# Kernel optimization log

Hardware: AMD Instinct MI355X
Metric: run time of the kernel (lower is better)

The kernel has to match this reference:

```python
import jax, jax.numpy as jnp
import numpy as np
from jax import lax

PI = jnp.pi
KX = jnp.array([[-1, 0, 1], [-2, 0, 2], [-1, 0, 1]], jnp.float32)
KY = jnp.array([[-1, -2, -1], [0, 0, 0], [1, 2, 1]], jnp.float32)
K45 = jnp.array([[-2, -1, 0], [-1, 0, 1], [0, 1, 2]], jnp.float32)
K135 = jnp.array([[0, 1, 2], [-1, 0, 1], [-2, -1, 0]], jnp.float32)


def _shift(x, dx, dy):
    # result[i, j] = x[clip(i - dx), clip(j - dy)]  (replicate boundary),
    # exactly matching the torch slice + replicate-pad neighbor construction.
    H, W = x.shape[2], x.shape[3]
    ri = jnp.clip(jnp.arange(H) - dx, 0, H - 1)
    ci = jnp.clip(jnp.arange(W) - dy, 0, W - 1)
    return x[:, :, ri[:, None], ci[None, :]]


def _adaptive_smoothing(f, k=10.0, iter_num=3):
    neighbors = [(-1, -1), (-1, 0), (-1, 1), (0, -1), (0, 0), (0, 1), (1, -1), (1, 0), (1, 1)]
    for _ in range(iter_num):
        Gx = (_shift(f, -1, 0) - _shift(f, 1, 0)) * 0.5   # gradient along H
        Gy = (_shift(f, 0, -1) - _shift(f, 0, 1)) * 0.5   # gradient along W
        w = jnp.exp(-(Gx * Gx + Gy * Gy) / (2.0 * k * k))
        f_new = jnp.zeros_like(f)
        w_sum = jnp.zeros_like(f)
        for dx, dy in neighbors:
            f_new = f_new + _shift(f, dx, dy) * _shift(w, dx, dy)
            w_sum = w_sum + _shift(w, dx, dy)
        f = f_new / jnp.maximum(w_sum, 1e-8)
    return f


def _dwconv(x, k2d):
    # depthwise 3x3 cross-correlation, zero padding (torch Conv2d semantics)
    C = x.shape[1]
    kern = jnp.broadcast_to(k2d[None, None], (C, 1, 3, 3)).astype(x.dtype)
    return lax.conv_general_dilated(x, kern, (1, 1), ((1, 1), (1, 1)),
                                    dimension_numbers=('NCHW', 'OIHW', 'NCHW'),
                                    feature_group_count=C)


def _sobel(x):
    return 0.5 * jnp.abs(_dwconv(x, KX)) + 0.5 * jnp.abs(_dwconv(x, KY))


def _hardswish(x):
    return x * jnp.clip(x + 3.0, 0.0, 6.0) / 6.0


def _canny(data, sigma, weight):
    blurred = _adaptive_smoothing(data, k=10.0, iter_num=3)
    sob = _sobel(blurred)
    B, C, H, W = sob.shape
    # torch.median: lower median = sorted[(n-1)//2]; .item() detaches it
    flat = jnp.sort(sob.reshape(B, C, H * W), axis=-1)
    med = lax.stop_gradient(jnp.mean(flat[:, :, (H * W - 1) // 2]))
    low = jnp.clip((1.0 - sigma) * med, 0.001, 1.0)
    high = jnp.clip((1.0 + sigma) * med, 0.001, 1.0)

    ex = _dwconv(blurred, KX)
    ey = _dwconv(blurred, KY)
    e45 = _dwconv(blurred, K45)
    e135 = _dwconv(blurred, K135)
    mag = jnp.sqrt(ex * ex + ey * ey + e45 * e45 + e135 * e135)
    ang = jnp.mod(jnp.arctan2(ey, ex), PI)

    dirs = jnp.array([0.0, PI / 4, PI / 2, 3 * PI / 4], jnp.float32)
    d = jnp.abs(ang[..., None] - dirs)
    dir_w = jax.nn.softmax(-jnp.minimum(d, PI - d) / 0.01, axis=-1)  # (B,C,H,W,4)

    pm = jnp.pad(mag, ((0, 0), (0, 0), (1, 1), (1, 1)), mode='edge')
    neigh = [(pm[:, :, 1:-1, :-2], pm[:, :, 1:-1, 2:]),
             (pm[:, :, :-2, :-2], pm[:, :, 2:, 2:]),
             (pm[:, :, :-2, 1:-1], pm[:, :, 2:, 1:-1]),
             (pm[:, :, :-2, 2:], pm[:, :, 2:, :-2])]
    sup = jnp.zeros_like(mag)
    for i, (n1, n2) in enumerate(neigh):  # fixed 4-direction loop
        sw = jax.nn.softmax(jnp.stack([mag, n1, n2], axis=-1) / 0.1, axis=-1)[..., 0]
        sup = sup + mag * sw * dir_w[..., i]

    mx = jnp.max(sup)
    sup = sup / jnp.where(mx > 0, mx, 1.0)

    Sh = _hardswish(sup - high)
    Sl = _hardswish(sup - low)
    ecanny = sup * (Sh + Sl)
    dilated = _dwconv(Sh, jnp.ones((3, 3), jnp.float32))
    result = ecanny + dilated * Sl * (1.0 - Sh)

    # enhance_edges with the ORIGINAL input
    result = (1.0 - weight) * result + weight * _sobel(data)
    rmin = jnp.min(result)
    rmax = jnp.max(result)
    return (result - rmin) / (rmax - rmin)


def setup_inputs() -> dict:
    key = jax.random.key(0)
    k1, k2 = jax.random.split(key)
    B, C, H, W = 8, 1, 512, 512
    return {
        'img1': jax.random.uniform(k1, (B, C, H, W), dtype=jnp.float32),
        'img2': jax.random.uniform(k2, (B, C, H, W), dtype=jnp.float32),
        'sigma1': jnp.float32(2.2),
        'enhance_weight1': jnp.float32(0.0),
        'sigma2': jnp.float32(2.2),
        'enhance_weight2': jnp.float32(0.0),
    }


def reference(img1, img2, sigma1, enhance_weight1, sigma2, enhance_weight2):
    s1 = 1.0 - jax.nn.sigmoid(sigma1)
    w1 = jax.nn.sigmoid(enhance_weight1)
    s2 = 1.0 - jax.nn.sigmoid(sigma2)
    w2 = jax.nn.sigmoid(enhance_weight2)
    m1 = _canny(img1, s1, w1)
    m2 = _canny(img2, s2, w2)
    f = (1.0 - m1) * (1.0 - m2) + m1 * m2
    return (1.0 - f, m1, m2)
```

## Files before the change

kernel.cpp:

```cpp
#include <hip/hip_runtime.h>

namespace {

constexpr int H = 512;
constexpr int W = 512;
constexpr int HW = H * W;
constexpr int PPS = 8;
constexpr int NP = 16;
constexpr int TX = 64;
constexpr int TY = 16;
constexpr int STY = 16;
constexpr int NBLK = (W / TX) * (H / TY) * NP;
constexpr int HBLK = NBLK / 2;
constexpr float PI_F = 3.14159265358979323846f;
constexpr int NBINS = 1024;
constexpr float BIN_SCALE = 512.0f;

__device__ __forceinline__ float hsw(float x) {
    float t = fminf(fmaxf(x + 3.0f, 0.0f), 6.0f);
    return x * t * (1.0f / 6.0f);
}

__device__ __forceinline__ const float* plane_ptr(const float* s1, const float* s2, int p) {
    return (p < PPS) ? (s1 + (size_t)p * HW) : (s2 + (size_t)(p - PPS) * HW);
}

__device__ __forceinline__ float wave_max(float v) {
    for (int o = 32; o > 0; o >>= 1) v = fmaxf(v, __shfl_down(v, o, 64));
    return v;
}
__device__ __forceinline__ float wave_min(float v) {
    for (int o = 32; o > 0; o >>= 1) v = fminf(v, __shfl_down(v, o, 64));
    return v;
}

__device__ __forceinline__ float atan_poly(float t) {
    float z = t * t;
    float p = -0.01172120f;
    p = p * z + 0.05265332f;
    p = p * z - 0.11643287f;
    p = p * z + 0.19354346f;
    p = p * z - 0.33262347f;
    p = p * z + 0.99997726f;
    return t * p;
}

__device__ __forceinline__ float sel4(int idx, float v0, float v1, float v2, float v3) {
    float a = (idx & 1) ? v1 : v0;
    float b = (idx & 1) ? v3 : v2;
    return (idx & 2) ? b : a;
}

__global__ void K_smooth(const float* __restrict__ s1, const float* __restrict__ s2,
                         float* __restrict__ fout, unsigned* __restrict__ hist) {
    int tid = threadIdx.y * 64 + threadIdx.x;
    if (hist) {
        int bid = (blockIdx.z * gridDim.y + blockIdx.y) * gridDim.x + blockIdx.x;
        if (bid < (NP * NBINS) / 256) hist[bid * 256 + tid] = 0;
    }
    int p = blockIdx.z;
    const float* f = plane_ptr(s1, s2, p);
    int j0 = blockIdx.x * 64, i0 = blockIdx.y * STY;
    __shared__ float fs[STY + 4][72];
    __shared__ float ws[STY + 2][66];

    bool interior = (i0 >= 2) && (i0 + STY + 1 <= H - 1) && (j0 >= 4) && (j0 + 67 <= W - 1);

    if (interior) {
        const float* fb = f + (i0 - 2) * W + (j0 - 4);
        for (int e = tid; e < (STY + 4) * 18; e += 256) {
            int y = e / 18, x4 = e % 18;
            float4 v = *(const float4*)(fb + y * W + x4 * 4);
            *(float4*)&fs[y][x4 * 4] = v;
        }
        __syncthreads();
        for (int e = tid; e < (STY + 2) * 66; e += 256) {
            int y = e / 66, x = e % 66;
            float gx = 0.5f * (fs[y + 2][x + 3] - fs[y][x + 3]);
            float gy = 0.5f * (fs[y + 1][x + 4] - fs[y + 1][x + 2]);
            ws[y][x] = __expf(-(gx * gx + gy * gy) * (1.0f / 200.0f));
        }
    } else {
        for (int e = tid; e < (STY + 4) * 72; e += 256) {
            int y = e / 72, x = e % 72;
            int gi = min(max(i0 - 2 + y, 0), H - 1);
            int gj = min(max(j0 - 4 + x, 0), W - 1);
            fs[y][x] = f[gi * W + gj];
        }
        __syncthreads();
        for (int e = tid; e < (STY + 2) * 66; e += 256) {
            int y = e / 66, x = e % 66;
            int r = min(max(i0 - 1 + y, 0), H - 1);
            int c = min(max(j0 - 1 + x, 0), W - 1);
            int yr = r - (i0 - 2), xc = c - (j0 - 4);
            int ym = max(r - 1, 0) - (i0 - 2), yp = min(r + 1, H - 1) - (i0 - 2);
            int xm = max(c - 1, 0) - (j0 - 4), xp = min(c + 1, W - 1) - (j0 - 4);
            float gx = 0.5f * (fs[yp][xc] - fs[ym][xc]);
            float gy = 0.5f * (fs[yr][xp] - fs[yr][xm]);
            ws[y][x] = __expf(-(gx * gx + gy * gy) * (1.0f / 200.0f));
        }
    }
    __syncthreads();

    int yl = threadIdx.y * 4;
    int xl = threadIdx.x;
    float rn[6], rd[6];
#pragma unroll
    for (int k = 0; k < 6; k++) {
        float w0 = ws[yl + k][xl], w1 = ws[yl + k][xl + 1], w2 = ws[yl + k][xl + 2];
        float fA = fs[yl + k + 1][xl + 3], fB = fs[yl + k + 1][xl + 4], fC = fs[yl + k + 1][xl + 5];
        rn[k] = fA * w0 + fB * w1 + fC * w2;
        rd[k] = w0 + w1 + w2;
    }
    size_t base = (size_t)p * HW + (i0 + yl) * W + (j0 + xl);
#pragma unroll
    for (int k = 0; k < 4; k++) {
        fout[base + (size_t)k * W] =
            (rn[k] + rn[k + 1] + rn[k + 2]) / fmaxf(rd[k] + rd[k + 1] + rd[k + 2], 1e-8f);
    }
}

__global__ void K_dnms(const float* __restrict__ blur, float* __restrict__ sup,
                       unsigned* __restrict__ hist, float* __restrict__ pmax) {
    int p = blockIdx.z;
    const float* f = blur + (size_t)p * HW;
    int j0 = blockIdx.x * TX, i0 = blockIdx.y * TY;
    __shared__ float fs0[TY + 4][72];
    __shared__ float ms[TY + 2][TX + 2];
    __shared__ unsigned histS[NBINS];
    __shared__ float wred[4];
    int tid = threadIdx.y * 64 + threadIdx.x;

    bool interior = (i0 >= 2) && (i0 + TY + 1 <= H - 1) && (j0 >= 4) && (j0 + 67 <= W - 1);

    for (int e = tid; e < NBINS; e += 256) histS[e] = 0;
    if (interior) {
        const float* fb = f + (i0 - 2) * W + (j0 - 4);
        for (int e = tid; e < (TY + 4) * 18; e += 256) {
            int y = e / 18, x4 = e % 18;
            float4 v = *(const float4*)(fb + y * W + x4 * 4);
            *(float4*)&fs0[y][x4 * 4] = v;
        }
    } else {
        for (int e = tid; e < (TY + 4) * 72; e += 256) {
            int y = e / 72, x = e % 72;
            int gi = i0 - 2 + y, gj = j0 - 4 + x;
            fs0[y][x] = (gi >= 0 && gi < H && gj >= 0 && gj < W) ? f[gi * W + gj] : 0.0f;
        }
    }
    __syncthreads();

    int xl = threadIdx.x;
    int yb = threadIdx.y * 4;

    float fv[6][3];
#pragma unroll
    for (int rr = 0; rr < 6; rr++)
#pragma unroll
        for (int cc = 0; cc < 3; cc++)
            fv[rr][cc] = fs0[yb + 1 + rr][xl + 3 + cc];

    float exk[4], eyk[4];
#pragma unroll
    for (int k = 0; k < 4; k++) {
        float xmm = fv[k][0], xm0 = fv[k][1], xmp = fv[k][2];
        float x0m = fv[k + 1][0], x0p = fv[k + 1][2];
        float xpm = fv[k + 2][0], xp0 = fv[k + 2][1], xpp = fv[k + 2][2];
        float ex = (xmp - xmm) + 2.0f * (x0p - x0m) + (xpp - xpm);
        float ey = (xpm + 2.0f * xp0 + xpp) - (xmm + 2.0f * xm0 + xmp);
        float e45 = -2.0f * xmm - xm0 - x0m + x0p + xp0 + 2.0f * xpp;
        float e135 = xm0 + 2.0f * xmp - x0m + x0p - 2.0f * xpm - xp0;
        ms[yb + 1 + k][xl + 1] = sqrtf(ex * ex + ey * ey + e45 * e45 + e135 * e135);
        exk[k] = ex;
        eyk[k] = ey;
    }

    if (tid < 2 * (TX + 2) + 2 * TY) {
        int y, x;
        if (tid < TX + 2) { y = 0; x = tid; }
        else if (tid < 2 * (TX + 2)) { y = TY + 1; x = tid - (TX + 2); }
        else if (tid < 2 * (TX + 2) + TY) { y = tid - 2 * (TX + 2) + 1; x = 0; }
        else { y = tid - (2 * (TX + 2) + TY) + 1; x = TX + 1; }
        int rr, cc;
        if (interior) { rr = y + 1; cc = x + 3; }
        else {
            int r = min(max(i0 - 1 + y, 0), H - 1);
            int c = min(max(j0 - 1 + x, 0), W - 1);
            rr = r - i0 + 2; cc = c - j0 + 4;
        }
        float xmm = fs0[rr - 1][cc - 1], xm0 = fs0[rr - 1][cc], xmp = fs0[rr - 1][cc + 1];
        float x0m = fs0[rr][cc - 1], x0p = fs0[rr][cc + 1];
        float xpm = fs0[rr + 1][cc - 1], xp0 = fs0[rr + 1][cc], xpp = fs0[rr + 1][cc + 1];
        float ex = (xmp - xmm) + 2.0f * (x0p - x0m) + (xpp - xpm);
        float ey = (xpm + 2.0f * xp0 + xpp) - (xmm + 2.0f * xm0 + xmp);
        float e45 = -2.0f * xmm - xm0 - x0m + x0p + xp0 + 2.0f * xpp;
        float e135 = xm0 + 2.0f * xmp - x0m + x0p - 2.0f * xpm - xp0;
        ms[y][x] = sqrtf(ex * ex + ey * ey + e45 * e45 + e135 * e135);
    }
    __syncthreads();

    float msr[6][3];
#pragma unroll
    for (int rr = 0; rr < 6; rr++)
#pragma unroll
        for (int cc = 0; cc < 3; cc++)
            msr[rr][cc] = ms[yb + rr][xl + cc];

    float bmax = 0.0f;
#pragma unroll
    for (int k = 0; k < 4; k++) {
        float ex = exk[k], ey = eyk[k];

        float ax = fabsf(ex), ay = fabsf(ey);
        float mn = fminf(ax, ay), mxv = fmaxf(ax, ay);
        float tq = (mxv > 0.0f) ? __fdividef(mn, mxv) : 0.0f;
        float pang = atan_poly(tq);
        if (ay > ax) pang = 1.57079632679f - pang;
        bool obtuse = ((__float_as_uint(ex) ^ __float_as_uint(ey)) & 0x80000000u) != 0u;
        float a = obtuse ? PI_F - pang : pang;

        float fa = a * 1.27323954474f;
        float nf = floorf(fa + 0.5f);
        float diff = a - nf * 0.78539816340f;
        float delta = fabsf(diff);
        int n = (int)nf & 3;
        int m = ((diff >= 0.0f) ? (int)nf + 1 : (int)nf - 1) & 3;
        float t = __expf(200.0f * delta - 78.5398163397f);
        float u = __fdividef(1.0f, 1.0f + t);

        float m0 = msr[k + 1][1];
        float n1a = msr[k + 1][0], n1b = msr[k][0], n1c = msr[k][1], n1d = msr[k][2];
        float n2a = msr[k + 1][2], n2b = msr[k + 2][2], n2c = msr[k + 2][1], n2d = msr[k + 2][0];
        float n1n = sel4(n, n1a, n1b, n1c, n1d);
        float n2n = sel4(n, n2a, n2b, n2c, n2d);
        float n1m = sel4(m, n1a, n1b, n1c, n1d);
        float n2m = sel4(m, n2a, n2b, n2c, n2d);

        float g1n = __expf((n1n - m0) * 10.0f);
        float g2n = __expf((n2n - m0) * 10.0f);
        float g1m = __expf((n1m - m0) * 10.0f);
        float g2m = __expf((n2m - m0) * 10.0f);
        float swn = __fdividef(1.0f, 1.0f + g1n + g2n);
        float swm = __fdividef(1.0f, 1.0f + g1m + g2m);
        float s = m0 * u * (swn + t * swm);

        sup[(size_t)p * HW + (i0 + yb + k) * W + (j0 + xl)] = s;
        bmax = fmaxf(bmax, s);

        float sv = 0.5f * (ax + ay);
        int bin = min((int)(sv * BIN_SCALE), NBINS - 1);
        atomicAdd(&histS[bin], 1u);
    }

    float wv = wave_max(bmax);
    if ((tid & 63) == 0) wred[tid >> 6] = wv;
    __syncthreads();
    if (tid == 0) {
        int bflat = (blockIdx.z * gridDim.y + blockIdx.y) * gridDim.x + blockIdx.x;
        pmax[bflat] = fmaxf(fmaxf(wred[0], wred[1]), fmaxf(wred[2], wred[3]));
    }
    for (int e = tid; e < NBINS; e += 256)
        if (histS[e]) atomicAdd(&hist[p * NBINS + e], histS[e]);
}

__global__ void K_stats(const unsigned* __restrict__ hist, const float* __restrict__ pmax,
                        float* __restrict__ medv, float* __restrict__ mx) {
    int b = blockIdx.x;
    int t = threadIdx.x;
    if (b < NP) {
        __shared__ unsigned sums[256];
        const unsigned* hp = hist + b * NBINS;
        unsigned s = 0;
        for (int q = 0; q < NBINS / 256; q++) s += hp[t * (NBINS / 256) + q];
        sums[t] = s;
        __syncthreads();
        for (int off = 1; off < 256; off <<= 1) {
            unsigned v = (t >= off) ? sums[t - off] : 0u;
            __syncthreads();
            sums[t] += v;
            __syncthreads();
        }
        const int k = (HW - 1) / 2;
        unsigned base = (t == 0) ? 0u : sums[t - 1];
        if ((int)base <= k && k < (int)sums[t]) {
            int cum = (int)base;
            int bin = t * (NBINS / 256);
            for (int q = 0; q < NBINS / 256; q++) {
                int c = (int)hp[t * (NBINS / 256) + q];
                if (cum + c > k) { bin = t * (NBINS / 256) + q; break; }
                cum += c;
            }
            medv[b] = ((float)bin + 0.5f) * (1.0f / BIN_SCALE);
        }
    } else {
        __shared__ float red[256];
        int s = b - NP;
        const float* base = pmax + s * HBLK;
        float v = -1e30f;
        for (int i = t; i < HBLK; i += 256) v = fmaxf(v, base[i]);
        red[t] = v;
        __syncthreads();
        for (int sft = 128; sft > 0; sft >>= 1) {
            if (t < sft) red[t] = fmaxf(red[t], red[t + sft]);
            __syncthreads();
        }
        if (t == 0) mx[s] = red[0];
    }
}

__global__ void K_result(const float* __restrict__ sup, const float* __restrict__ im1,
                         const float* __restrict__ im2, const float* __restrict__ medv,
                         const float* __restrict__ sg1, const float* __restrict__ ew1,
                         const float* __restrict__ sg2, const float* __restrict__ ew2,
                         const float* __restrict__ mx, float* __restrict__ res,
                         float* __restrict__ prmax, float* __restrict__ prmin) {
    int p = blockIdx.z;
    int s = p >> 3;
    float med = 0.125f * (medv[s * PPS + 0] + medv[s * PPS + 1] + medv[s * PPS + 2] +
                          medv[s * PPS + 3] + medv[s * PPS + 4] + medv[s * PPS + 5] +
                          medv[s * PPS + 6] + medv[s * PPS + 7]);
    float sgin = (s == 0) ? sg1[0] : sg2[0];
    float ewin = (s == 0) ? ew1[0] : ew2[0];
    float sig = 1.0f - 1.0f / (1.0f + __expf(-sgin));
    float lo = fminf(fmaxf((1.0f - sig) * med, 0.001f), 1.0f);
    float hi = fminf(fmaxf((1.0f + sig) * med, 0.001f), 1.0f);
    float wg = 1.0f / (1.0f + __expf(-ewin));
    float m = mx[s];
    float inv = 1.0f / ((m > 0.0f) ? m : 1.0f);

    const float* sp = sup + (size_t)p * HW;
    const float* op = plane_ptr(im1, im2, p);
    int j0 = blockIdx.x * TX, i0 = blockIdx.y * TY;
    __shared__ float hs2[TY + 2][72];
    __shared__ float og[TY + 2][72];
    __shared__ float ssn[TY][TX];
    __shared__ float wredx[4], wredn[4];
    int tid = threadIdx.y * 64 + threadIdx.x;

    bool interior = (i0 >= 1) && (i0 + TY <= H - 1) && (j0 >= 4) && (j0 + 67 <= W - 1);

    if (interior) {
        const float* spb = sp + (i0 - 1) * W + (j0 - 4);
        const float* opb = op + (i0 - 1) * W + (j0 - 4);
        for (int e = tid; e < (TY + 2) * 18; e += 256) {
            int y = e / 18, x4 = e % 18;
            float4 a = *(const float4*)(spb + y * W + x4 * 4);
            float4 o = *(const float4*)(opb + y * W + x4 * 4);
            float sv0 = a.x * inv, sv1 = a.y * inv, sv2 = a.z * inv, sv3 = a.w * inv;
            float4 hv;
            hv.x = hsw(sv0 - hi); hv.y = hsw(sv1 - hi);
            hv.z = hsw(sv2 - hi); hv.w = hsw(sv3 - hi);
            *(float4*)&hs2[y][x4 * 4] = hv;
            *(float4*)&og[y][x4 * 4] = o;
            if (y >= 1 && y <= TY) {
                int c0 = x4 * 4;
                if (c0 + 0 >= 4 && c0 + 0 <= 67) ssn[y - 1][c0 - 4] = sv0;
                if (c0 + 1 >= 4 && c0 + 1 <= 67) ssn[y - 1][c0 - 3] = sv1;
                if (c0 + 2 >= 4 && c0 + 2 <= 67) ssn[y - 1][c0 - 2] = sv2;
                if (c0 + 3 >= 4 && c0 + 3 <= 67) ssn[y - 1][c0 - 1] = sv3;
            }
        }
    } else {
        for (int e = tid; e < (TY + 2) * 72; e += 256) {
            int y = e / 72, x = e % 72;
            int gi = i0 - 1 + y, gj = j0 - 4 + x;
            float h = 0.0f, o = 0.0f;
            if (gi >= 0 && gi < H && gj >= 0 && gj < W) {
                float sv = sp[gi * W + gj] * inv;
                h = hsw(sv - hi);
                o = op[gi * W + gj];
                if (y >= 1 && y <= TY && x >= 4 && x <= 67) ssn[y - 1][x - 4] = sv;
            }
            hs2[y][x] = h;
            og[y][x] = o;
        }
    }
    __syncthreads();

    int yl = threadIdx.y * 4;
    int xl = threadIdx.x;
    float hrow[6], ddr[6], ssr[6];
#pragma unroll
    for (int k = 0; k < 6; k++) {
        float a = hs2[yl + k][xl + 3], bq = hs2[yl + k][xl + 4], c = hs2[yl + k][xl + 5];
        hrow[k] = a + bq + c;
        float oa = og[yl + k][xl + 3], ob = og[yl + k][xl + 4], oc = og[yl + k][xl + 5];
        ddr[k] = oc - oa;
        ssr[k] = oa + 2.0f * ob + oc;
    }

    float bmx = -1e30f, bmn = 1e30f;
    size_t gbase = (size_t)p * HW + (i0 + yl) * W + (j0 + xl);
#pragma unroll
    for (int k = 0; k < 4; k++) {
        float sn = ssn[yl + k][xl];
        float Sh = hs2[yl + k + 1][xl + 4];
        float Sl = hsw(sn - lo);
        float dil = hrow[k] + hrow[k + 1] + hrow[k + 2];
        float pre = sn * (Sh + Sl) + dil * Sl * (1.0f - Sh);
        float sob = 0.5f * fabsf(ddr[k] + 2.0f * ddr[k + 1] + ddr[k + 2]) +
                    0.5f * fabsf(ssr[k + 2] - ssr[k]);
        float r = (1.0f - wg) * pre + wg * sob;
        res[gbase + (size_t)k * W] = r;
        bmx = fmaxf(bmx, r);
        bmn = fminf(bmn, r);
    }

    float vx = wave_max(bmx), vn = wave_min(bmn);
    if ((tid & 63) == 0) { wredx[tid >> 6] = vx; wredn[tid >> 6] = vn; }
    __syncthreads();
    if (tid == 0) {
        int bflat = (blockIdx.z * gridDim.y + blockIdx.y) * gridDim.x + blockIdx.x;
        prmax[bflat] = fmaxf(fmaxf(wredx[0], wredx[1]), fmaxf(wredx[2], wredx[3]));
        prmin[bflat] = fminf(fminf(wredn[0], wredn[1]), fminf(wredn[2], wredn[3]));
    }
}

__global__ void K_final(const float* __restrict__ res, const float* __restrict__ prmax,
                        const float* __restrict__ prmin, float* __restrict__ out) {
    int tid = threadIdx.y * 64 + threadIdx.x;

    float vx0 = -1e30f, vn0 = 1e30f, vx1 = -1e30f, vn1 = 1e30f;
    for (int i = tid; i < HBLK; i += 256) {
        vx0 = fmaxf(vx0, prmax[i]);
        vn0 = fminf(vn0, prmin[i]);
        vx1 = fmaxf(vx1, prmax[HBLK + i]);
        vn1 = fminf(vn1, prmin[HBLK + i]);
    }
    vx0 = wave_max(vx0); vn0 = wave_min(vn0);
    vx1 = wave_max(vx1); vn1 = wave_min(vn1);
    __shared__ float sx0[4], sn0[4], sx1[4], sn1[4];
    if ((tid & 63) == 0) {
        int w = tid >> 6;
        sx0[w] = vx0; sn0[w] = vn0; sx1[w] = vx1; sn1[w] = vn1;
    }
    __syncthreads();
    float mx1 = fmaxf(fmaxf(sx0[0], sx0[1]), fmaxf(sx0[2], sx0[3]));
    float mn1 = fminf(fminf(sn0[0], sn0[1]), fminf(sn0[2], sn0[3]));
    float mx2 = fmaxf(fmaxf(sx1[0], sx1[1]), fmaxf(sx1[2], sx1[3]));
    float mn2 = fminf(fminf(sn1[0], sn1[1]), fminf(sn1[2], sn1[3]));
    float is1 = 1.0f / (mx1 - mn1);
    float is2 = 1.0f / (mx2 - mn2);

    int col4 = blockIdx.x * 64 + threadIdx.x;
    int i0 = blockIdx.y * 16 + threadIdx.y * 4;
    int p = blockIdx.z;
    const float4* r1p = (const float4*)(res + (size_t)p * HW);
    const float4* r2p = (const float4*)(res + (size_t)(p + PPS) * HW);
    float4* outc = (float4*)(out) + (size_t)p * (HW / 4);
    float4* out1 = (float4*)(out) + (size_t)(PPS + p) * (HW / 4);
    float4* out2 = (float4*)(out) + (size_t)(2 * PPS + p) * (HW / 4);

#pragma unroll
    for (int k = 0; k < 4; k++) {
        int row = i0 + k;
        float4 a = r1p[row * (W / 4) + col4];
        float4 b = r2p[row * (W / 4) + col4];
        float4 m1v, m2v, mcv;
        m1v.x = (a.x - mn1) * is1; m1v.y = (a.y - mn1) * is1;
        m1v.z = (a.z - mn1) * is1; m1v.w = (a.w - mn1) * is1;
        m2v.x = (b.x - mn2) * is2; m2v.y = (b.y - mn2) * is2;
        m2v.z = (b.z - mn2) * is2; m2v.w = (b.w - mn2) * is2;
        mcv.x = m1v.x + m2v.x - 2.0f * m1v.x * m2v.x;
        mcv.y = m1v.y + m2v.y - 2.0f * m1v.y * m2v.y;
        mcv.z = m1v.z + m2v.z - 2.0f * m1v.z * m2v.z;
        mcv.w = m1v.w + m2v.w - 2.0f * m1v.w * m2v.w;
        outc[row * (W / 4) + col4] = mcv;
        out1[row * (W / 4) + col4] = m1v;
        out2[row * (W / 4) + col4] = m2v;
    }
}

}

extern "C" void kernel_launch(void* const* d_in, const int* in_sizes, int n_in,
                              void* d_out, int out_size, void* d_ws, size_t ws_size,
                              hipStream_t stream) {
    const float* img1 = (const float*)d_in[0];
    const float* img2 = (const float*)d_in[1];
    const float* sg1 = (const float*)d_in[2];
    const float* ew1 = (const float*)d_in[3];
    const float* sg2 = (const float*)d_in[4];
    const float* ew2 = (const float*)d_in[5];
    float* out = (float*)d_out;

    float* A = (float*)d_ws;
    float* B = A + (size_t)NP * HW;
    float* C = B + (size_t)NP * HW;
    unsigned* hist = (unsigned*)(C + (size_t)NP * HW);
    float* medv = (float*)(hist + NP * NBINS);
    float* mx = medv + NP;
    float* pmax = mx + 2;
    float* prmax = pmax + NBLK;
    float* prmin = prmax + NBLK;

    dim3 blk(64, 4, 1);
    dim3 grdT(W / TX, H / TY, NP);
    dim3 grdS(W / 64, H / STY, NP);
    dim3 grdF(W / 256, H / 16, PPS);
    dim3 mblk(256, 1, 1);

    K_smooth<<<grdS, blk, 0, stream>>>(img1, img2, A, hist);
    K_smooth<<<grdS, blk, 0, stream>>>(A, A + (size_t)PPS * HW, B, nullptr);
    K_smooth<<<grdS, blk, 0, stream>>>(B, B + (size_t)PPS * HW, A, nullptr);

    K_dnms<<<grdT, blk, 0, stream>>>(A, C, hist, pmax);

    K_stats<<<dim3(NP + 2), mblk, 0, stream>>>(hist, pmax, medv, mx);

    K_result<<<grdT, blk, 0, stream>>>(C, img1, img2, medv, sg1, ew1, sg2, ew2, mx,
                                       B, prmax, prmin);

    K_final<<<grdF, blk, 0, stream>>>(B, prmax, prmin, out);
}
```

Measured before the change: 109.8 us.

## Fuse first two adaptive smoothing iterations into one kernel with halo recompute

Adds K_smooth2, which loads a wider 4-pixel halo tile and runs two adaptive-smoothing iterations back to back in shared memory, recomputing the overlapping halo region. This replaces two of the three smoothing launches, removing one full-plane global write and read plus a launch. In exchange it does redundant halo compute, uses more shared memory per block, and adds extra barriers, which may lower occupancy.

```diff
diff --git a/kernel.cpp b/kernel.cpp
--- a/kernel.cpp
+++ b/kernel.cpp
@@ -51,13 +51,131 @@
     return (idx & 2) ? b : a;
 }
 
-__global__ void K_smooth(const float* __restrict__ s1, const float* __restrict__ s2,
-                         float* __restrict__ fout, unsigned* __restrict__ hist) {
+__global__ void K_smooth2(const float* __restrict__ s1, const float* __restrict__ s2,
+                          float* __restrict__ fout, unsigned* __restrict__ hist) {
     int tid = threadIdx.y * 64 + threadIdx.x;
     if (hist) {
         int bid = (blockIdx.z * gridDim.y + blockIdx.y) * gridDim.x + blockIdx.x;
         if (bid < (NP * NBINS) / 256) hist[bid * 256 + tid] = 0;
     }
+    int p = blockIdx.z;
+    const float* f = plane_ptr(s1, s2, p);
+    int j0 = blockIdx.x * 64, i0 = blockIdx.y * STY;
+    __shared__ float fs0[24][72];
+    __shared__ float w1b[23][72];
+    __shared__ float f1b[20][72];
+
+    bool interior = (i0 >= 4) && (i0 + STY + 3 <= H - 1) && (j0 >= 4) && (j0 + 67 <= W - 1);
+
+    if (interior) {
+        const float* fb = f + (i0 - 4) * W + (j0 - 4);
+        for (int e = tid; e < 24 * 18; e += 256) {
+            int y = e / 18, x4 = e % 18;
+            *(float4*)&fs0[y][x4 * 4] = *(const float4*)(fb + y * W + x4 * 4);
+        }
+        __syncthreads();
+        for (int e = tid; e < 22 * 70; e += 256) {
+            int a = 1 + e / 70, b = 1 + e % 70;
+            float gx = 0.5f * (fs0[a + 1][b] - fs0[a - 1][b]);
+            float gy = 0.5f * (fs0[a][b + 1] - fs0[a][b - 1]);
+            w1b[a][b] = __expf(-(gx * gx + gy * gy) * (1.0f / 200.0f));
+        }
+        __syncthreads();
+        for (int e = tid; e < 20 * 68; e += 256) {
+            int a = 2 + e / 68, b = 2 + e % 68;
+            float num = fs0[a - 1][b - 1] * w1b[a - 1][b - 1] + fs0[a - 1][b] * w1b[a - 1][b] +
+                        fs0[a - 1][b + 1] * w1b[a - 1][b + 1] + fs0[a][b - 1] * w1b[a][b - 1] +
+                        fs0[a][b] * w1b[a][b] + fs0[a][b + 1] * w1b[a][b + 1] +
+                        fs0[a + 1][b - 1] * w1b[a + 1][b - 1] + fs0[a + 1][b] * w1b[a + 1][b] +
+                        fs0[a + 1][b + 1] * w1b[a + 1][b + 1];
+            float den = w1b[a - 1][b - 1] + w1b[a - 1][b] + w1b[a - 1][b + 1] +
+                        w1b[a][b - 1] + w1b[a][b] + w1b[a][b + 1] +
+                        w1b[a + 1][b - 1] + w1b[a + 1][b] + w1b[a + 1][b + 1];
+            f1b[a - 2][b] = num / fmaxf(den, 1e-8f);
+        }
+        __syncthreads();
+        for (int e = tid; e < 18 * 66; e += 256) {
+            int a = 3 + e / 66, b = 3 + e % 66;
+            float gx = 0.5f * (f1b[a - 1][b] - f1b[a - 3][b]);
+            float gy = 0.5f * (f1b[a - 2][b + 1] - f1b[a - 2][b - 1]);
+            w1b[a][b] = __expf(-(gx * gx + gy * gy) * (1.0f / 200.0f));
+        }
+    } else {
+        for (int e = tid; e < 24 * 72; e += 256) {
+            int y = e / 72, x = e % 72;
+            int gi = min(max(i0 - 4 + y, 0), H - 1);
+            int gj = min(max(j0 - 4 + x, 0), W - 1);
+            fs0[y][x] = f[gi * W + gj];
+        }
+        __syncthreads();
+        for (int e = tid; e < 22 * 70; e += 256) {
+            int a = 1 + e / 70, b = 1 + e % 70;
+            int r = min(max(i0 - 4 + a, 0), H - 1);
+            int c = min(max(j0 - 4 + b, 0), W - 1);
+            int rr = r - (i0 - 4), cc = c - (j0 - 4);
+            int rm = max(r - 1, 0) - (i0 - 4), rp = min(r + 1, H - 1) - (i0 - 4);
+            int cm = max(c - 1, 0) - (j0 - 4), cp = min(c + 1, W - 1) - (j0 - 4);
+            float gx = 0.5f * (fs0[rp][cc] - fs0[rm][cc]);
+            float gy = 0.5f * (fs0[rr][cp] - fs0[rr][cm]);
+            w1b[a][b] = __expf(-(gx * gx + gy * gy) * (1.0f / 200.0f));
+        }
+        __syncthreads();
+        for (int e = tid; e < 20 * 68; e += 256) {
+            int a = 2 + e / 68, b = 2 + e % 68;
+            int r = min(max(i0 - 4 + a, 0), H - 1);
+            int c = min(max(j0 - 4 + b, 0), W - 1);
+            int ra1 = r - (i0 - 4);
+            int ra0 = max(r - 1, 0) - (i0 - 4);
+            int ra2 = min(r + 1, H - 1) - (i0 - 4);
+            int cb1 = c - (j0 - 4);
+            int cb0 = max(c - 1, 0) - (j0 - 4);
+            int cb2 = min(c + 1, W - 1) - (j0 - 4);
+            float num = fs0[ra0][cb0] * w1b[ra0][cb0] + fs0[ra0][cb1] * w1b[ra0][cb1] +
+                        fs0[ra0][cb2] * w1b[ra0][cb2] + fs0[ra1][cb0] * w1b[ra1][cb0] +
+                        fs0[ra1][cb1] * w1b[ra1][cb1] + fs0[ra1][cb2] * w1b[ra1][cb2] +
+                        fs0[ra2][cb0] * w1b[ra2][cb0] + fs0[ra2][cb1] * w1b[ra2][cb1] +
+                        fs0[ra2][cb2] * w1b[ra2][cb2];
+            float den = w1b[ra0][cb0] + w1b[ra0][cb1] + w1b[ra0][cb2] +
+                        w1b[ra1][cb0] + w1b[ra1][cb1] + w1b[ra1][cb2] +
+                        w1b[ra2][cb0] + w1b[ra2][cb1] + w1b[ra2][cb2];
+            f1b[a - 2][b] = num / fmaxf(den, 1e-8f);
+        }
+        __syncthreads();
+        for (int e = tid; e < 18 * 66; e += 256) {
+            int a = 3 + e / 66, b = 3 + e % 66;
+            int r = min(max(i0 - 4 + a, 0), H - 1);
+            int c = min(max(j0 - 4 + b, 0), W - 1);
+            int rr = r - (i0 - 4) - 2, cc = c - (j0 - 4);
+            int rm = max(r - 1, 0) - (i0 - 4) - 2, rp = min(r + 1, H - 1) - (i0 - 4) - 2;
+            int cm = max(c - 1, 0) - (j0 - 4), cp = min(c + 1, W - 1) - (j0 - 4);
+            float gx = 0.5f * (f1b[rp][cc] - f1b[rm][cc]);
+            float gy = 0.5f * (f1b[rr][cp] - f1b[rr][cm]);
+            w1b[a][b] = __expf(-(gx * gx + gy * gy) * (1.0f / 200.0f));
+        }
+    }
+    __syncthreads();
+
+    int yl = threadIdx.y * 4;
+    int xl = threadIdx.x;
+    float rn[6], rd[6];
+#pragma unroll
+    for (int kk = 0; kk < 6; kk++) {
+        float wv0 = w1b[3 + yl + kk][xl + 3], wv1 = w1b[3 + yl + kk][xl + 4], wv2 = w1b[3 + yl + kk][xl + 5];
+        float fA = f1b[1 + yl + kk][xl + 3], fB = f1b[1 + yl + kk][xl + 4], fC = f1b[1 + yl + kk][xl + 5];
+        rn[kk] = fA * wv0 + fB * wv1 + fC * wv2;
+        rd[kk] = wv0 + wv1 + wv2;
+    }
+    size_t base = (size_t)p * HW + (i0 + yl) * W + (j0 + xl);
+#pragma unroll
+    for (int k = 0; k < 4; k++) {
+        fout[base + (size_t)k * W] =
+            (rn[k] + rn[k + 1] + rn[k + 2]) / fmaxf(rd[k] + rd[k + 1] + rd[k + 2], 1e-8f);
+    }
+}
+
+__global__ void K_smooth(const float* __restrict__ s1, const float* __restrict__ s2,
+                         float* __restrict__ fout) {
+    int tid = threadIdx.y * 64 + threadIdx.x;
     int p = blockIdx.z;
     const float* f = plane_ptr(s1, s2, p);
     int j0 = blockIdx.x * 64, i0 = blockIdx.y * STY;
@@ -500,9 +618,8 @@
     dim3 grdF(W / 256, H / 16, PPS);
     dim3 mblk(256, 1, 1);
 
-    K_smooth<<<grdS, blk, 0, stream>>>(img1, img2, A, hist);
-    K_smooth<<<grdS, blk, 0, stream>>>(A, A + (size_t)PPS * HW, B, nullptr);
-    K_smooth<<<grdS, blk, 0, stream>>>(B, B + (size_t)PPS * HW, A, nullptr);
+    K_smooth2<<<grdS, blk, 0, stream>>>(img1, img2, B, hist);
+    K_smooth<<<grdS, blk, 0, stream>>>(B, B + (size_t)PPS * HW, A);
 
     K_dnms<<<grdT, blk, 0, stream>>>(A, C, hist, pmax);
 
```

New measurement: 113.4 us. +3.3%, slower.
